# Kernel tuning notes

Hardware: AMD Instinct MI355X
Metric: run time of the kernel (lower is better)

The kernel has to match this reference:

```python
import jax, jax.numpy as jnp
import numpy as np
import math

PAD = 0
EPS = 1e-5


def _mha(x, ids, num_heads, qw, qb, kw, kb, vw, vb, pw, pb):
    # Faithful vectorization of the per-head Python loop: identical math per head.
    B, S, D = x.shape
    d = D // num_heads
    q = (x @ qw + qb).reshape(B, S, num_heads, d)
    k = (x @ kw + kb).reshape(B, S, num_heads, d)
    v = (x @ vw + vb).reshape(B, S, num_heads, d)
    scores = jnp.einsum('bqhd,bkhd->bhqk', q, k) / math.sqrt(d)
    key_mask = (ids != PAD)[:, None, None, :]  # mask padded KEYS only (as in source)
    scores = jnp.where(key_mask, scores, -jnp.inf)
    w = jax.nn.softmax(scores, axis=-1)
    out = jnp.einsum('bhqk,bkhd->bqhd', w, v).reshape(B, S, D)
    return out @ pw + pb + x  # projection + residual


def setup_inputs() -> dict:
    V, D, B, S = 50257, 1024, 64, 512
    key = jax.random.key(0)
    ks = jax.random.split(key, 24)
    s = 0.02

    def lin(k, din, dout):
        k1, k2 = jax.random.split(k)
        return (jax.random.normal(k1, (din, dout), jnp.float32) * s,
                jax.random.normal(k2, (dout,), jnp.float32) * s)

    x = jax.random.randint(ks[0], (B, S), 0, V, dtype=jnp.int64)
    emb_w = jax.random.normal(ks[1], (V, D), jnp.float32) * s
    pos_w = jax.random.normal(ks[2], (512, D), jnp.float32) * s
    a1_qw, a1_qb = lin(ks[3], D, D)
    a1_kw, a1_kb = lin(ks[4], D, D)
    a1_vw, a1_vb = lin(ks[5], D, D)
    a1_pw, a1_pb = lin(ks[6], D, D)
    a2_qw, a2_qb = lin(ks[7], D, D)
    a2_kw, a2_kb = lin(ks[8], D, D)
    a2_vw, a2_vb = lin(ks[9], D, D)
    a2_pw, a2_pb = lin(ks[10], D, D)
    norm_g = jnp.ones((D,), jnp.float32)
    norm_b = jnp.zeros((D,), jnp.float32)
    lin_w, lin_b = lin(ks[11], D, 1)
    return dict(x=x, emb_w=emb_w, pos_w=pos_w,
                a1_qw=a1_qw, a1_qb=a1_qb, a1_kw=a1_kw, a1_kb=a1_kb,
                a1_vw=a1_vw, a1_vb=a1_vb, a1_pw=a1_pw, a1_pb=a1_pb,
                a2_qw=a2_qw, a2_qb=a2_qb, a2_kw=a2_kw, a2_kb=a2_kb,
                a2_vw=a2_vw, a2_vb=a2_vb, a2_pw=a2_pw, a2_pb=a2_pb,
                norm_g=norm_g, norm_b=norm_b, lin_w=lin_w, lin_b=lin_b)


def reference(x, emb_w, pos_w,
              a1_qw, a1_qb, a1_kw, a1_kb, a1_vw, a1_vb, a1_pw, a1_pb,
              a2_qw, a2_qb, a2_kw, a2_kb, a2_vw, a2_vb, a2_pw, a2_pb,
              norm_g, norm_b, lin_w, lin_b):
    B, S = x.shape
    h = emb_w[x] + pos_w[jnp.arange(S)][None, :, :]  # word + positional emb
    res_emb = h
    h = _mha(h, x, 8, a1_qw, a1_qb, a1_kw, a1_kb, a1_vw, a1_vb, a1_pw, a1_pb)
    # dropout is identity in eval
    h = _mha(h, x, 4, a2_qw, a2_qb, a2_kw, a2_kb, a2_vw, a2_vb, a2_pw, a2_pb)
    h = h + res_emb
    # mean pooling over non-pad tokens (type=0 branch)
    m = (x != PAD)[:, :, None].astype(h.dtype)
    pooled = jnp.sum(h * m, axis=1) / jnp.sum(m, axis=1)
    # LayerNorm
    mu = jnp.mean(pooled, axis=-1, keepdims=True)
    var = jnp.mean((pooled - mu) ** 2, axis=-1, keepdims=True)
    normed = (pooled - mu) / jnp.sqrt(var + EPS) * norm_g + norm_b
    return normed @ lin_w + lin_b  # [B, 1]
```

## Files before the change

kernel.cpp:

```cpp
#include <hip/hip_runtime.h>

typedef unsigned short u16;
typedef short short8 __attribute__((ext_vector_type(8)));
typedef float f32x4 __attribute__((ext_vector_type(4)));
typedef const __attribute__((address_space(1))) void* gptr_t;
typedef __attribute__((address_space(3))) void* lptr_t;

#define B_  64
#define S_  512
#define D_  1024
#define BS_ (B_*S_)

__device__ __forceinline__ float b2f(u16 v) {
    union { float f; unsigned u; } c; c.u = ((unsigned)v) << 16; return c.f;
}
__device__ __forceinline__ u16 f2b(float f) {
    union { float f; unsigned u; } c; c.f = f;
    unsigned r = c.u + 0x7FFFu + ((c.u >> 16) & 1u);
    return (u16)(r >> 16);
}

__global__ void detect_k(const u16* __restrict__ raw, int* __restrict__ flag) {
    __shared__ int cnt;
    if (threadIdx.x == 0) cnt = 0;
    __syncthreads();
    u16 v = raw[threadIdx.x * 2];
    int e = (v >> 7) & 0xFF;
    int sane = (e >= 64 && e <= 150) ? 1 : 0;
    atomicAdd(&cnt, sane);
    __syncthreads();
    if (threadIdx.x == 0) *flag = (cnt >= 192) ? 1 : 0;
}

__global__ __launch_bounds__(256) void convert_params_k(
    const void* b0, const void* b1, const void* b2, const void* b3,
    const void* b4, const void* b5, const void* b6, const void* b7,
    const void* g, const void* be, const void* lw, const void* lb,
    const int* __restrict__ flagp, u16* __restrict__ dst)
{
    const void* srcs[12] = {b0, b1, b2, b3, b4, b5, b6, b7, g, be, lw, lb};
    int slot = blockIdx.x;
    int n = (slot == 11) ? 1 : 1024;
    int f = *flagp;
    const void* s = srcs[slot];
    for (int i = threadIdx.x; i < n; i += 256) {
        float v = f ? b2f(((const u16*)s)[i]) : ((const float*)s)[i];
        dst[slot * 1024 + i] = f2b(v);
    }
}

__global__ __launch_bounds__(256) void transpose_k(const void* __restrict__ W,
                                                   u16* __restrict__ Wt,
                                                   const int* __restrict__ flagp) {
    __shared__ float t[32][33];
    int f = *flagp;
    int tx = threadIdx.x, ty = threadIdx.y;
    int x0 = blockIdx.x * 32, y0 = blockIdx.y * 32;
    for (int i = ty; i < 32; i += 8) {
        size_t idx = (size_t)(y0 + i) * D_ + x0 + tx;
        t[i][tx] = f ? b2f(((const u16*)W)[idx]) : ((const float*)W)[idx];
    }
    __syncthreads();
    for (int i = ty; i < 32; i += 8)
        Wt[(size_t)(x0 + i) * D_ + y0 + tx] = f2b(t[tx][i]);
}

__global__ __launch_bounds__(256) void embed_k(const int* __restrict__ x, const void* __restrict__ emb,
                                               const void* __restrict__ pos, u16* __restrict__ h0,
                                               const int* __restrict__ flagp) {
    int f = *flagp;
    int bs = blockIdx.x;
    int s = bs & (S_ - 1);
    int tok = x[bs];
    u16* orow = h0 + (size_t)bs * D_;
    int c = threadIdx.x * 4;
    float e0, e1, e2, e3, p0, p1, p2, p3;
    if (f) {
        ushort4 e = *(const ushort4*)((const u16*)emb + (size_t)tok * D_ + c);
        ushort4 p = *(const ushort4*)((const u16*)pos + (size_t)s * D_ + c);
        e0 = b2f(e.x); e1 = b2f(e.y); e2 = b2f(e.z); e3 = b2f(e.w);
        p0 = b2f(p.x); p1 = b2f(p.y); p2 = b2f(p.z); p3 = b2f(p.w);
    } else {
        float4 e = *(const float4*)((const float*)emb + (size_t)tok * D_ + c);
        float4 p = *(const float4*)((const float*)pos + (size_t)s * D_ + c);
        e0 = e.x; e1 = e.y; e2 = e.z; e3 = e.w;
        p0 = p.x; p1 = p.y; p2 = p.z; p3 = p.w;
    }
    ushort4 o;
    o.x = f2b(e0 + p0); o.y = f2b(e1 + p1); o.z = f2b(e2 + p2); o.w = f2b(e3 + p3);
    *(ushort4*)(orow + c) = o;
}

template <int NT>
__global__ __launch_bounds__(512, 2) void gemm256_k(
    const u16* __restrict__ A, const u16* __restrict__ Bt,
    const u16* __restrict__ bias,
    const u16* __restrict__ res, const u16* __restrict__ res2,
    u16* __restrict__ Cq, u16* __restrict__ Ck, u16* __restrict__ Vt)
{
    int bid = blockIdx.x;
    int xcd = bid & 7;
    int loc = bid >> 3;
    int chunk = loc >> 6;
    int r = loc & 63;
    int mt = xcd * 16 + (r >> 2);
    int nt = chunk * 4 + (r & 3);
    int m0 = mt * 256, n0 = nt * 256;

    int tid = threadIdx.x;
    int lane = tid & 63, wid = tid >> 6, quad = lane >> 4, l16 = lane & 15;
    int wm = wid >> 2, wn = wid & 3;
    int pxor = l16 & 7;

    __shared__ __align__(16) u16 lds[2][2][2][128 * 64];

    f32x4 acc[8][4];
#pragma unroll
    for (int i = 0; i < 8; i++)
#pragma unroll
        for (int j = 0; j < 4; j++) acc[i][j] = (f32x4){0.f, 0.f, 0.f, 0.f};

    int srow = tid >> 3;
    int skof = ((tid & 7) ^ (srow & 7)) * 8;

    auto STAGE_KT = [&](int kt) {
        int p = kt & 1;
        int kbase = kt * 64;
#pragma unroll
        for (int hh = 0; hh < 4; ++hh) {
            int mat = hh >> 1, hlf = hh & 1;
            const u16* src = (mat == 0)
                ? A  + (size_t)(m0 + hlf * 128) * D_ + kbase
                : Bt + (size_t)(n0 + hlf * 128) * D_ + kbase;
            u16* dst = &lds[p][mat][hlf][0];
            __builtin_amdgcn_global_load_lds((gptr_t)(src + (size_t)srow * D_ + skof),
                                             (lptr_t)(dst + tid * 8), 16, 0, 0);
            __builtin_amdgcn_global_load_lds((gptr_t)(src + (size_t)(srow + 64) * D_ + skof),
                                             (lptr_t)(dst + 4096 + tid * 8), 16, 0, 0);
        }
    };

    STAGE_KT(0);
    asm volatile("s_waitcnt vmcnt(0)" ::: "memory");
    __builtin_amdgcn_s_barrier();

    int brow0 = (wn & 1) * 64;
    for (int kt = 0; kt < 16; ++kt) {
        int p = kt & 1;
        if (kt < 15) STAGE_KT(kt + 1);

        const u16* Ah = &lds[p][0][wm][0];
        const u16* Bh = &lds[p][1][wn >> 1][0];

        short8 bf[4][2];
#pragma unroll
        for (int nj = 0; nj < 4; ++nj)
#pragma unroll
            for (int kh = 0; kh < 2; ++kh)
                bf[nj][kh] = *(const short8*)&Bh[(brow0 + nj * 16 + l16) * 64 +
                                                 ((kh * 4 + quad) ^ pxor) * 8];
#pragma unroll
        for (int q = 0; q < 4; ++q) {
            short8 af[2][2];
#pragma unroll
            for (int mi2 = 0; mi2 < 2; ++mi2)
#pragma unroll
                for (int kh = 0; kh < 2; ++kh)
                    af[mi2][kh] = *(const short8*)&Ah[((2 * q + mi2) * 16 + l16) * 64 +
                                                      ((kh * 4 + quad) ^ pxor) * 8];
            __builtin_amdgcn_s_setprio(1);
#pragma unroll
            for (int kh = 0; kh < 2; ++kh)
#pragma unroll
                for (int mi2 = 0; mi2 < 2; ++mi2)
#pragma unroll
                    for (int nj = 0; nj < 4; ++nj)
                        acc[2 * q + mi2][nj] = __builtin_amdgcn_mfma_f32_16x16x32_bf16(
                            af[mi2][kh], bf[nj][kh], acc[2 * q + mi2][nj], 0, 0, 0);
            __builtin_amdgcn_s_setprio(0);
        }
        if (kt < 15) {
            asm volatile("s_waitcnt vmcnt(0)" ::: "memory");
            __builtin_amdgcn_s_barrier();
        }
    }

#pragma unroll
    for (int mi = 0; mi < 8; ++mi) {
        int rowb = m0 + wm * 128 + mi * 16 + quad * 4;
#pragma unroll
        for (int nj = 0; nj < 4; ++nj) {
            int col = n0 + wn * 64 + nj * 16 + l16;
            float bv = b2f(bias[col]);
            bool vpath = (NT == 12) && (col >= 2048);
            if (vpath) {
                int colv = col - 2048;
                int bb = rowb >> 9, sbase = rowb & (S_ - 1);
                u16* dst = Vt + ((size_t)bb * D_ + colv) * S_ + sbase;
                ushort4 pk;
                pk.x = f2b(acc[mi][nj][0] + bv);
                pk.y = f2b(acc[mi][nj][1] + bv);
                pk.z = f2b(acc[mi][nj][2] + bv);
                pk.w = f2b(acc[mi][nj][3] + bv);
                *(ushort4*)dst = pk;
            } else {
                u16* Cd = (NT == 12 && col >= 1024) ? Ck : Cq;
                int colc = col & 1023;
#pragma unroll
                for (int rr = 0; rr < 4; ++rr) {
                    size_t idx = (size_t)(rowb + rr) * D_ + colc;
                    float v = acc[mi][nj][rr] + bv;
                    if (res)  v += b2f(res[idx]);
                    if (res2) v += b2f(res2[idx]);
                    Cd[idx] = f2b(v);
                }
            }
        }
    }
}

template <int HD>
__global__ __launch_bounds__(512, HD == 128 ? 4 : 2) void attn4_k(
    const u16* Q, const u16* __restrict__ Kn, const u16* __restrict__ Vt,
    const int* __restrict__ x, u16* O, int H)
{
    constexpr int NKF = HD / 32, NOF = HD / 16;
    constexpr int KP = HD + 8;
    constexpr int VP = 40;
    constexpr int KC = (32 * HD / 8) / 512;
    constexpr int VC = (HD * 32 / 8) / 512;
    const float scale = (HD == 128) ? 0.08838834764831845f : 0.0625f;
    int bh = blockIdx.x;
    int b = bh / H, h = bh - b * H;
    int tid = threadIdx.x, wid = tid >> 6, lane = tid & 63, quad = lane >> 4, l16 = lane & 15;
    int qrow = blockIdx.y * 128 + wid * 16;

    const u16* Qb = Q + (size_t)(b * S_) * D_ + h * HD;
    const u16* Kb = Kn + (size_t)(b * S_) * D_ + h * HD;
    const u16* Vb = Vt + ((size_t)b * D_ + h * HD) * S_;
    const int* xb = x + b * S_;

    __shared__ __align__(16) u16 Ks[32 * KP];
    __shared__ __align__(16) u16 Vs[HD * VP];
    __shared__ __align__(16) u16 Pl[8 * 16 * 32];

    short8 qf[NKF];
#pragma unroll
    for (int f = 0; f < NKF; ++f)
        qf[f] = *(const short8*)(Qb + (size_t)(qrow + l16) * D_ + f * 32 + quad * 8);

    f32x4 of[NOF];
    float lpart[4];
#pragma unroll
    for (int f = 0; f < NOF; ++f) of[f] = (f32x4){0.f, 0.f, 0.f, 0.f};
#pragma unroll
    for (int r = 0; r < 4; ++r) lpart[r] = 0.f;

    short8 kreg[KC], vreg[VC];
    auto LOADKV = [&](int key0) {
#pragma unroll
        for (int i = 0; i < KC; ++i) {
            int c = tid + i * 512;
            int row = c / (HD / 8), col = (c % (HD / 8)) * 8;
            kreg[i] = *(const short8*)(Kb + (size_t)(key0 + row) * D_ + col);
        }
#pragma unroll
        for (int i = 0; i < VC; ++i) {
            int c = tid + i * 512;
            int row = c >> 2, col = (c & 3) * 8;
            vreg[i] = *(const short8*)(Vb + (size_t)row * S_ + key0 + col);
        }
    };

    LOADKV(0);

    for (int key0 = 0; key0 < S_; key0 += 32) {
        __syncthreads();
#pragma unroll
        for (int i = 0; i < KC; ++i) {
            int c = tid + i * 512;
            int row = c / (HD / 8), col = (c % (HD / 8)) * 8;
            *(short8*)&Ks[row * KP + col] = kreg[i];
        }
#pragma unroll
        for (int i = 0; i < VC; ++i) {
            int c = tid + i * 512;
            int row = c >> 2, col = (c & 3) * 8;
            *(short8*)&Vs[row * VP + col] = vreg[i];
        }
        if (key0 + 32 < S_) LOADKV(key0 + 32);
        int tok0 = xb[key0 + l16] != 0;
        int tok1 = xb[key0 + 16 + l16] != 0;
        __syncthreads();

        f32x4 sc0 = (f32x4){0.f, 0.f, 0.f, 0.f};
        f32x4 sc1 = (f32x4){0.f, 0.f, 0.f, 0.f};
#pragma unroll
        for (int f = 0; f < NKF; ++f) {
            short8 k0 = *(const short8*)&Ks[l16 * KP + f * 32 + quad * 8];
            short8 k1 = *(const short8*)&Ks[(16 + l16) * KP + f * 32 + quad * 8];
            sc0 = __builtin_amdgcn_mfma_f32_16x16x32_bf16(qf[f], k0, sc0, 0, 0, 0);
            sc1 = __builtin_amdgcn_mfma_f32_16x16x32_bf16(qf[f], k1, sc1, 0, 0, 0);
        }
#pragma unroll
        for (int r = 0; r < 4; ++r) {
            float p0 = tok0 ? __expf(sc0[r] * scale) : 0.f;
            float p1 = tok1 ? __expf(sc1[r] * scale) : 0.f;
            lpart[r] += p0 + p1;
            Pl[wid * 512 + (quad * 4 + r) * 32 + l16] = f2b(p0);
            Pl[wid * 512 + (quad * 4 + r) * 32 + 16 + l16] = f2b(p1);
        }
        __asm volatile("s_waitcnt lgkmcnt(0)" ::: "memory");
        short8 pf = *(const short8*)&Pl[wid * 512 + l16 * 32 + quad * 8];
#pragma unroll
        for (int f = 0; f < NOF; ++f) {
            short8 vf = *(const short8*)&Vs[(f * 16 + l16) * VP + quad * 8];
            of[f] = __builtin_amdgcn_mfma_f32_16x16x32_bf16(pf, vf, of[f], 0, 0, 0);
        }
    }

    u16* Ob = O + (size_t)(b * S_) * D_ + h * HD;
    float rl[4];
#pragma unroll
    for (int r = 0; r < 4; ++r) {
        float l = lpart[r];
#pragma unroll
        for (int msk = 1; msk < 16; msk <<= 1) l += __shfl_xor(l, msk, 64);
        rl[r] = 1.0f / l;
    }
#pragma unroll
    for (int f = 0; f < NOF; ++f)
#pragma unroll
        for (int r = 0; r < 4; ++r)
            Ob[(size_t)(qrow + quad * 4 + r) * D_ + f * 16 + l16] =
                f2b(of[f][r] * rl[r]);
}

__global__ __launch_bounds__(256) void pool_zero_k(float* __restrict__ pooled, int* __restrict__ cnt) {
    int b = blockIdx.x;
    for (int i = threadIdx.x; i < 1024; i += 256) pooled[b * 1024 + i] = 0.f;
    if (threadIdx.x == 0) cnt[b] = 0;
}

__global__ __launch_bounds__(256) void pool_partial_k(
    const u16* __restrict__ Hf, const int* __restrict__ x,
    float* __restrict__ pooled, int* __restrict__ cnt)
{
    int b = blockIdx.x, seg = blockIdx.y;
    int c = threadIdx.x * 4;
    const int* xb = x + b * S_;
    float a0 = 0.f, a1 = 0.f, a2 = 0.f, a3 = 0.f;
    int local = 0;
    int s0 = seg * 64;
    for (int i = 0; i < 64; ++i) {
        int s = s0 + i;
        if (xb[s] != 0) {
            ushort4 hv = *(const ushort4*)(Hf + (size_t)(b * S_ + s) * D_ + c);
            a0 += b2f(hv.x); a1 += b2f(hv.y); a2 += b2f(hv.z); a3 += b2f(hv.w);
            local++;
        }
    }
    atomicAdd(&pooled[b * 1024 + c + 0], a0);
    atomicAdd(&pooled[b * 1024 + c + 1], a1);
    atomicAdd(&pooled[b * 1024 + c + 2], a2);
    atomicAdd(&pooled[b * 1024 + c + 3], a3);
    if (threadIdx.x == 0) atomicAdd(&cnt[b], local);
}

__global__ __launch_bounds__(256) void pool_final_k(
    const float* __restrict__ pooled, const int* __restrict__ cnt,
    const u16* __restrict__ prm, void* __restrict__ out, const int* __restrict__ flagp)
{
    __shared__ float sb[8];
    const u16* g  = prm + 8 * 1024;
    const u16* be = prm + 9 * 1024;
    const u16* lw = prm + 10 * 1024;
    const u16* lb = prm + 11 * 1024;
    int b = blockIdx.x;
    int c = threadIdx.x * 4;
    int n = cnt[b];
    float inv = 1.0f / (float)(n > 0 ? n : 1);
    float p0 = pooled[b * 1024 + c + 0] * inv;
    float p1 = pooled[b * 1024 + c + 1] * inv;
    float p2 = pooled[b * 1024 + c + 2] * inv;
    float p3 = pooled[b * 1024 + c + 3] * inv;
    float s1 = p0 + p1 + p2 + p3;
    float s2 = p0 * p0 + p1 * p1 + p2 * p2 + p3 * p3;
#pragma unroll
    for (int m = 32; m >= 1; m >>= 1) { s1 += __shfl_xor(s1, m, 64); s2 += __shfl_xor(s2, m, 64); }
    int wid = threadIdx.x >> 6, lane = threadIdx.x & 63;
    if (lane == 0) { sb[wid] = s1; sb[4 + wid] = s2; }
    __syncthreads();
    float S1 = sb[0] + sb[1] + sb[2] + sb[3];
    float S2 = sb[4] + sb[5] + sb[6] + sb[7];
    float mu = S1 * (1.0f / 1024.0f);
    float var = S2 * (1.0f / 1024.0f) - mu * mu;
    float rstd = rsqrtf(var + 1e-5f);
    float dot = ((p0 - mu) * rstd * b2f(g[c + 0]) + b2f(be[c + 0])) * b2f(lw[c + 0])
              + ((p1 - mu) * rstd * b2f(g[c + 1]) + b2f(be[c + 1])) * b2f(lw[c + 1])
              + ((p2 - mu) * rstd * b2f(g[c + 2]) + b2f(be[c + 2])) * b2f(lw[c + 2])
              + ((p3 - mu) * rstd * b2f(g[c + 3]) + b2f(be[c + 3])) * b2f(lw[c + 3]);
#pragma unroll
    for (int m = 32; m >= 1; m >>= 1) dot += __shfl_xor(dot, m, 64);
    __syncthreads();
    if (lane == 0) sb[wid] = dot;
    __syncthreads();
    if (threadIdx.x == 0) {
        float v = sb[0] + sb[1] + sb[2] + sb[3] + b2f(lb[0]);
        if (*flagp) ((u16*)out)[b] = f2b(v);
        else        ((float*)out)[b] = v;
    }
}

extern "C" void kernel_launch(void* const* d_in, const int* in_sizes, int n_in,
                              void* d_out, int out_size, void* d_ws, size_t ws_size,
                              hipStream_t stream)
{
    (void)in_sizes; (void)n_in; (void)out_size; (void)ws_size;
    const int* x = (const int*)d_in[0];

    char* ws = (char*)d_ws;
    size_t off = 0;
    auto carve = [&](size_t bytes) -> char* {
        char* p = ws + off;
        off += (bytes + 255) & ~(size_t)255;
        return p;
    };
    int* flag    = (int*)carve(256);
    u16* prm     = (u16*)carve(12 * 1024 * 2);
    float* pooled = (float*)carve(64 * 1024 * 4);
    int* cnt     = (int*)carve(64 * 4);
    const size_t WB = (size_t)D_ * D_ * 2;
    const size_t HB = (size_t)BS_ * D_ * 2;
    u16* wt[8];
    for (int i = 0; i < 8; i++) wt[i] = (u16*)carve(WB);
    u16* h0   = (u16*)carve(HB);
    u16* buf2 = (u16*)carve(HB);
    u16* buf3 = (u16*)carve(HB);
    u16* buf4 = (u16*)carve(HB);
    u16* buf5 = (u16*)carve(HB);

    detect_k<<<1, 256, 0, stream>>>((const u16*)d_in[1], flag);
    convert_params_k<<<12, 256, 0, stream>>>(
        d_in[4], d_in[6], d_in[8], d_in[10], d_in[12], d_in[14], d_in[16], d_in[18],
        d_in[19], d_in[20], d_in[21], d_in[22], flag, prm);

    dim3 tb(32, 8), tg(32, 32);
    const int widx[8] = {3, 5, 7, 9, 11, 13, 15, 17};
    for (int i = 0; i < 8; i++)
        transpose_k<<<tg, tb, 0, stream>>>(d_in[widx[i]], wt[i], flag);

    embed_k<<<BS_, 256, 0, stream>>>(x, d_in[1], d_in[2], h0, flag);

    gemm256_k<12><<<1536, 512, 0, stream>>>(h0, wt[0], prm + 0 * 1024,
                                            nullptr, nullptr, buf2, buf3, buf4);
    attn4_k<128><<<dim3(B_ * 8, 4), 512, 0, stream>>>(buf2, buf3, buf4, x, buf2, 8);
    gemm256_k<4><<<512, 512, 0, stream>>>(buf2, wt[3], prm + 3 * 1024,
                                          h0, nullptr, buf5, nullptr, nullptr);
    gemm256_k<12><<<1536, 512, 0, stream>>>(buf5, wt[4], prm + 4 * 1024,
                                            nullptr, nullptr, buf2, buf3, buf4);
    attn4_k<256><<<dim3(B_ * 4, 4), 512, 0, stream>>>(buf2, buf3, buf4, x, buf2, 4);
    gemm256_k<4><<<512, 512, 0, stream>>>(buf2, wt[7], prm + 7 * 1024,
                                          buf5, h0, buf3, nullptr, nullptr);

    pool_zero_k<<<B_, 256, 0, stream>>>(pooled, cnt);
    pool_partial_k<<<dim3(B_, 8), 256, 0, stream>>>(buf3, x, pooled, cnt);
    pool_final_k<<<B_, 256, 0, stream>>>(pooled, cnt, prm, d_out, flag);
}
```

Measured before the change: 1.175 ms.

## Deepen GEMM main loop to a four-buffer K=32 pipeline with partial waits

Replaces the two-buffer K=64 staging in gemm256_k with four LDS buffers of K=32, keeping three stages of global-to-LDS loads in flight. Each iteration waits with a partial vmcnt instead of draining all loads, so memory latency overlaps more with MFMA work. The LDS swizzle is redone for 32-wide rows. Total LDS footprint is unchanged, but there are twice as many barriers per tile and fewer MFMAs between each sync.

```diff
diff --git a/kernel.cpp b/kernel.cpp
--- a/kernel.cpp
+++ b/kernel.cpp
@@ -110,9 +110,8 @@
     int tid = threadIdx.x;
     int lane = tid & 63, wid = tid >> 6, quad = lane >> 4, l16 = lane & 15;
     int wm = wid >> 2, wn = wid & 3;
-    int pxor = l16 & 7;
-
-    __shared__ __align__(16) u16 lds[2][2][2][128 * 64];
+
+    __shared__ __align__(16) u16 lds[4][2][256 * 32];
 
     f32x4 acc[8][4];
 #pragma unroll
@@ -120,70 +119,64 @@
 #pragma unroll
         for (int j = 0; j < 4; j++) acc[i][j] = (f32x4){0.f, 0.f, 0.f, 0.f};
 
-    int srow = tid >> 3;
-    int skof = ((tid & 7) ^ (srow & 7)) * 8;
-
-    auto STAGE_KT = [&](int kt) {
-        int p = kt & 1;
-        int kbase = kt * 64;
-#pragma unroll
-        for (int hh = 0; hh < 4; ++hh) {
-            int mat = hh >> 1, hlf = hh & 1;
-            const u16* src = (mat == 0)
-                ? A  + (size_t)(m0 + hlf * 128) * D_ + kbase
-                : Bt + (size_t)(n0 + hlf * 128) * D_ + kbase;
-            u16* dst = &lds[p][mat][hlf][0];
-            __builtin_amdgcn_global_load_lds((gptr_t)(src + (size_t)srow * D_ + skof),
-                                             (lptr_t)(dst + tid * 8), 16, 0, 0);
-            __builtin_amdgcn_global_load_lds((gptr_t)(src + (size_t)(srow + 64) * D_ + skof),
-                                             (lptr_t)(dst + 4096 + tid * 8), 16, 0, 0);
+    int srow0 = tid >> 2;
+    int skof  = (((tid & 3) ^ ((tid >> 3) & 3)) * 8);
+
+    auto STAGE = [&](int s) {
+        int buf = s & 3;
+        int kbase = s * 32;
+#pragma unroll
+        for (int l = 0; l < 2; ++l) {
+            int row = l * 128 + srow0;
+            const u16* srcA = A  + (size_t)(m0 + row) * D_ + kbase + skof;
+            const u16* srcB = Bt + (size_t)(n0 + row) * D_ + kbase + skof;
+            __builtin_amdgcn_global_load_lds((gptr_t)srcA,
+                (lptr_t)(&lds[buf][0][0] + l * 4096 + tid * 8), 16, 0, 0);
+            __builtin_amdgcn_global_load_lds((gptr_t)srcB,
+                (lptr_t)(&lds[buf][1][0] + l * 4096 + tid * 8), 16, 0, 0);
         }
     };
 
-    STAGE_KT(0);
+    auto COMPUTE = [&](int buf) {
+        const u16* Ah = &lds[buf][0][0];
+        const u16* Bh = &lds[buf][1][0];
+        short8 bf[4], af[8];
+#pragma unroll
+        for (int nj = 0; nj < 4; ++nj) {
+            int rB = wn * 64 + nj * 16 + l16;
+            bf[nj] = *(const short8*)&Bh[rB * 32 + ((quad ^ ((rB >> 1) & 3)) * 8)];
+        }
+#pragma unroll
+        for (int mi = 0; mi < 8; ++mi) {
+            int rA = wm * 128 + mi * 16 + l16;
+            af[mi] = *(const short8*)&Ah[rA * 32 + ((quad ^ ((rA >> 1) & 3)) * 8)];
+        }
+        __builtin_amdgcn_s_setprio(1);
+#pragma unroll
+        for (int mi = 0; mi < 8; ++mi)
+#pragma unroll
+            for (int nj = 0; nj < 4; ++nj)
+                acc[mi][nj] = __builtin_amdgcn_mfma_f32_16x16x32_bf16(
+                    af[mi], bf[nj], acc[mi][nj], 0, 0, 0);
+        __builtin_amdgcn_s_setprio(0);
+    };
+
+    STAGE(0); STAGE(1); STAGE(2);
+    for (int s = 0; s < 29; ++s) {
+        asm volatile("s_waitcnt vmcnt(8)" ::: "memory");
+        __builtin_amdgcn_s_barrier();
+        COMPUTE(s & 3);
+        STAGE(s + 3);
+    }
+    asm volatile("s_waitcnt vmcnt(8)" ::: "memory");
+    __builtin_amdgcn_s_barrier();
+    COMPUTE(29 & 3);
+    asm volatile("s_waitcnt vmcnt(4)" ::: "memory");
+    __builtin_amdgcn_s_barrier();
+    COMPUTE(30 & 3);
     asm volatile("s_waitcnt vmcnt(0)" ::: "memory");
     __builtin_amdgcn_s_barrier();
-
-    int brow0 = (wn & 1) * 64;
-    for (int kt = 0; kt < 16; ++kt) {
-        int p = kt & 1;
-        if (kt < 15) STAGE_KT(kt + 1);
-
-        const u16* Ah = &lds[p][0][wm][0];
-        const u16* Bh = &lds[p][1][wn >> 1][0];
-
-        short8 bf[4][2];
-#pragma unroll
-        for (int nj = 0; nj < 4; ++nj)
-#pragma unroll
-            for (int kh = 0; kh < 2; ++kh)
-                bf[nj][kh] = *(const short8*)&Bh[(brow0 + nj * 16 + l16) * 64 +
-                                                 ((kh * 4 + quad) ^ pxor) * 8];
-#pragma unroll
-        for (int q = 0; q < 4; ++q) {
-            short8 af[2][2];
-#pragma unroll
-            for (int mi2 = 0; mi2 < 2; ++mi2)
-#pragma unroll
-                for (int kh = 0; kh < 2; ++kh)
-                    af[mi2][kh] = *(const short8*)&Ah[((2 * q + mi2) * 16 + l16) * 64 +
-                                                      ((kh * 4 + quad) ^ pxor) * 8];
-            __builtin_amdgcn_s_setprio(1);
-#pragma unroll
-            for (int kh = 0; kh < 2; ++kh)
-#pragma unroll
-                for (int mi2 = 0; mi2 < 2; ++mi2)
-#pragma unroll
-                    for (int nj = 0; nj < 4; ++nj)
-                        acc[2 * q + mi2][nj] = __builtin_amdgcn_mfma_f32_16x16x32_bf16(
-                            af[mi2][kh], bf[nj][kh], acc[2 * q + mi2][nj], 0, 0, 0);
-            __builtin_amdgcn_s_setprio(0);
-        }
-        if (kt < 15) {
-            asm volatile("s_waitcnt vmcnt(0)" ::: "memory");
-            __builtin_amdgcn_s_barrier();
-        }
-    }
+    COMPUTE(31 & 3);
 
 #pragma unroll
     for (int mi = 0; mi < 8; ++mi) {
```

Result: slower. 1.210 ms (+3.0%).
